# Optimization experiments

Hardware: AMD Instinct MI355X
Metric: run time of the kernel (lower is better)

The kernel has to match this reference:

```python
import jax, jax.numpy as jnp
import numpy as np

N, IN_DIM, OUT_DIM = 8192, 256, 64
NEG_BIG = -9e15
LRELU_SLOPE = 0.01  # torch F.leaky_relu default


def setup_inputs() -> dict:
    key = jax.random.key(0)
    k1, k2, k3, k4 = jax.random.split(key, 4)
    inp = jax.random.normal(k1, (N, IN_DIM), dtype=jnp.float32)
    adj = jax.random.randint(k2, (N, N), 0, 2, dtype=jnp.int32)
    # xavier_uniform with gain=1.414
    limW = 1.414 * np.sqrt(6.0 / (IN_DIM + OUT_DIM))
    W = jax.random.uniform(k3, (IN_DIM, OUT_DIM), minval=-limW, maxval=limW, dtype=jnp.float32)
    lima = 1.414 * np.sqrt(6.0 / (2 * OUT_DIM + 1))
    a = jax.random.uniform(k4, (2 * OUT_DIM, 1), minval=-lima, maxval=lima, dtype=jnp.float32)
    return {"input": inp, "adj": adj, "W": W, "a": a}


def reference(input, adj, W, a):
    h = input @ W                      # [N, D]
    a1, a2 = a[:OUT_DIM, 0], a[OUT_DIM:, 0]
    # e[i,j] = leaky_relu(a1.h_i + a2.h_j) == the concat-based score, no NxNx2D tensor
    f1 = h @ a1                        # [N]
    f2 = h @ a2                        # [N]
    e = jax.nn.leaky_relu(f1[:, None] + f2[None, :], negative_slope=LRELU_SLOPE)  # [N, N]
    face_Rhand = e[1, 2]
    face_Lhand = e[1, 3]
    Rhand_Lhand = e[3, 2]
    attention = jnp.where(adj > 0, e, jnp.float32(NEG_BIG))
    alpha = jax.nn.softmax(attention, axis=1)
    h_prime = alpha @ h                # [N, D]
    return (h_prime, face_Rhand, face_Lhand, Rhand_Lhand)
```

## Files before the change

### kernel.cpp

```cpp
#include <hip/hip_runtime.h>
#include <hip/hip_bf16.h>

#define GN 8192
#define KD 256
#define OD 64
#define LOG2E 1.44269504f
#define ASTR 260
#define NCH 16

typedef __attribute__((ext_vector_type(8))) short bf16x8;
typedef __attribute__((ext_vector_type(4))) float f32x4;

__device__ __forceinline__ float fexp2(float x) {
#if __has_builtin(__builtin_amdgcn_exp2f)
  return __builtin_amdgcn_exp2f(x);
#else
  return exp2f(x);
#endif
}

__global__ __launch_bounds__(256) void gat_k1(
    const float* __restrict__ input, const float* __restrict__ W,
    const float* __restrict__ a, __hip_bfloat16* __restrict__ hTt,
    float* __restrict__ f1p, float* __restrict__ f2p, float* __restrict__ out)
{
  __shared__ float Wl[KD * OD];
  __shared__ float inT[KD * 33];
  __shared__ float red1[8][32];
  __shared__ float red2[8][32];
  __shared__ float s1row[32];
  __shared__ float s2row[32];

  const int tid = threadIdx.x;
  const int i0 = blockIdx.x * 32;

  for (int idx = tid; idx < KD * OD / 4; idx += 256)
    ((float4*)Wl)[idx] = ((const float4*)W)[idx];

#pragma unroll
  for (int it = 0; it < 8; ++it) {
    int idx = tid + it * 256;
    int r = idx >> 6, k4 = idx & 63;
    float4 v = *(const float4*)(input + (long)(i0 + r) * KD + k4 * 4);
    inT[(k4 * 4 + 0) * 33 + r] = v.x;
    inT[(k4 * 4 + 1) * 33 + r] = v.y;
    inT[(k4 * 4 + 2) * 33 + r] = v.z;
    inT[(k4 * 4 + 3) * 33 + r] = v.w;
  }
  __syncthreads();

  const int r = tid & 31;
  const int cg = tid >> 5;
  float acc[8];
#pragma unroll
  for (int c = 0; c < 8; ++c) acc[c] = 0.f;

#pragma unroll 4
  for (int k = 0; k < KD; ++k) {
    float inv = inT[k * 33 + r];
    float4 wa = *(const float4*)&Wl[k * 64 + cg * 8];
    float4 wb = *(const float4*)&Wl[k * 64 + cg * 8 + 4];
    acc[0] += inv * wa.x; acc[1] += inv * wa.y;
    acc[2] += inv * wa.z; acc[3] += inv * wa.w;
    acc[4] += inv * wb.x; acc[5] += inv * wb.y;
    acc[6] += inv * wb.z; acc[7] += inv * wb.w;
  }

#pragma unroll
  for (int c = 0; c < 8; ++c)
    hTt[(long)blockIdx.x * (OD * 32) + (cg * 8 + c) * 32 + r] =
        __float2bfloat16(acc[c]);

  float s1 = 0.f, s2 = 0.f;
#pragma unroll
  for (int c = 0; c < 8; ++c) {
    s1 += acc[c] * a[cg * 8 + c];
    s2 += acc[c] * a[OD + cg * 8 + c];
  }
  red1[cg][r] = s1; red2[cg][r] = s2;
  __syncthreads();
  if (tid < 32) {
    float f1 = 0.f, f2 = 0.f;
#pragma unroll
    for (int g = 0; g < 8; ++g) { f1 += red1[g][tid]; f2 += red2[g][tid]; }
    s1row[tid] = f1; s2row[tid] = f2;
    f1p[i0 + tid] = f1 * LOG2E;
    f2p[i0 + tid] = f2 * LOG2E;
  }
  __syncthreads();
  if (blockIdx.x == 0 && tid == 0) {
    float e12 = s1row[1] + s2row[2];
    float e13 = s1row[1] + s2row[3];
    float e32 = s1row[3] + s2row[2];
    out[(long)GN * OD + 0] = fmaxf(e12, 0.01f * e12);
    out[(long)GN * OD + 1] = fmaxf(e13, 0.01f * e13);
    out[(long)GN * OD + 2] = fmaxf(e32, 0.01f * e32);
  }
}

__global__ __launch_bounds__(256, 3) void gat_k2(
    const int* __restrict__ adj, const __hip_bfloat16* __restrict__ hTt,
    const float* __restrict__ f1p, const float* __restrict__ f2p,
    float* __restrict__ pn, float* __restrict__ pd)
{
  __shared__ int abuf[2][16 * ASTR];
  __shared__ float f2l[4096];
  float* pb = (float*)abuf;
  float* sb = pb + 4 * 16 * 68;

  const int tid = threadIdx.x;
  const int lane = tid & 63;
  const int wv = tid >> 6;
  const int tn = lane & 15;
  const int quad = lane >> 4;
  const int rg = blockIdx.x >> 1;
  const int js = blockIdx.x & 1;
  const int i0 = rg * 16;
  const int jbase = js * 4096;

  for (int i = tid; i < 4096 / 4; i += 256)
    ((float4*)f2l)[i] = ((const float4*)(f2p + jbase))[i];

  const float f1r = f1p[i0 + tn];

  const int sr = tid >> 4;
  const int sc = (tid & 15) * 4;
  const int* gsrc = adj + (long)(i0 + sr) * GN + jbase + sc;

  const int jo0 = wv * 64 + quad * 8;
  const int jo1 = jo0 + 32;
  const __hip_bfloat16* hsl = hTt + (long)(jbase / 32) * (OD * 32) + tn * 32 + quad * 8;

  f32x4 acc[4];
#pragma unroll
  for (int nf = 0; nf < 4; ++nf) acc[nf] = (f32x4){0.f, 0.f, 0.f, 0.f};
  f32x4 accS = (f32x4){0.f, 0.f, 0.f, 0.f};

  bf16x8 ones;
  {
    short ov = (tn == 0) ? (short)0x3F80 : (short)0;
#pragma unroll
    for (int i = 0; i < 8; ++i) ones[i] = ov;
  }

  int4 st[4];
#pragma unroll
  for (int k = 0; k < 4; ++k) st[k] = *(const int4*)(gsrc + 64 * k);
#pragma unroll
  for (int k = 0; k < 4; ++k) *(int4*)&abuf[0][sr * ASTR + sc + 64 * k] = st[k];
  __syncthreads();

  for (int c = 0; c < NCH; ++c) {
    const int cur = c & 1, nxt = cur ^ 1;

    const __hip_bfloat16* h0 = hsl + (long)(c * 8 + 2 * wv) * (OD * 32);
    const __hip_bfloat16* h1 = h0 + (OD * 32);
    bf16x8 B0[4], B1[4];
#pragma unroll
    for (int nf = 0; nf < 4; ++nf) {
      B0[nf] = *(const bf16x8*)(h0 + nf * (16 * 32));
      B1[nf] = *(const bf16x8*)(h1 + nf * (16 * 32));
    }

    if (c + 1 < NCH) {
#pragma unroll
      for (int k = 0; k < 4; ++k)
        st[k] = *(const int4*)(gsrc + (c + 1) * 256 + 64 * k);
    }

    const int4 a0 = *(const int4*)&abuf[cur][tn * ASTR + jo0];
    const int4 a1 = *(const int4*)&abuf[cur][tn * ASTR + jo0 + 4];
    const int4 a2 = *(const int4*)&abuf[cur][tn * ASTR + jo1];
    const int4 a3 = *(const int4*)&abuf[cur][tn * ASTR + jo1 + 4];
    const float4 f20 = *(const float4*)&f2l[c * 256 + jo0];
    const float4 f21 = *(const float4*)&f2l[c * 256 + jo0 + 4];
    const float4 f22 = *(const float4*)&f2l[c * 256 + jo1];
    const float4 f23 = *(const float4*)&f2l[c * 256 + jo1 + 4];

    union { bf16x8 v; unsigned u[4]; } w0, w1;
    {
      float e0 = f1r + f20.x, e1 = f1r + f20.y, e2 = f1r + f20.z, e3 = f1r + f20.w;
      float e4 = f1r + f21.x, e5 = f1r + f21.y, e6 = f1r + f21.z, e7 = f1r + f21.w;
      float v0 = fexp2((a0.x > 0) ? fmaxf(e0, 0.01f * e0) : -256.f);
      float v1 = fexp2((a0.y > 0) ? fmaxf(e1, 0.01f * e1) : -256.f);
      float v2 = fexp2((a0.z > 0) ? fmaxf(e2, 0.01f * e2) : -256.f);
      float v3 = fexp2((a0.w > 0) ? fmaxf(e3, 0.01f * e3) : -256.f);
      float v4 = fexp2((a1.x > 0) ? fmaxf(e4, 0.01f * e4) : -256.f);
      float v5 = fexp2((a1.y > 0) ? fmaxf(e5, 0.01f * e5) : -256.f);
      float v6 = fexp2((a1.z > 0) ? fmaxf(e6, 0.01f * e6) : -256.f);
      float v7 = fexp2((a1.w > 0) ? fmaxf(e7, 0.01f * e7) : -256.f);
      w0.u[0] = __builtin_amdgcn_perm(__float_as_uint(v1), __float_as_uint(v0), 0x07060302u);
      w0.u[1] = __builtin_amdgcn_perm(__float_as_uint(v3), __float_as_uint(v2), 0x07060302u);
      w0.u[2] = __builtin_amdgcn_perm(__float_as_uint(v5), __float_as_uint(v4), 0x07060302u);
      w0.u[3] = __builtin_amdgcn_perm(__float_as_uint(v7), __float_as_uint(v6), 0x07060302u);
    }
    {
      float e0 = f1r + f22.x, e1 = f1r + f22.y, e2 = f1r + f22.z, e3 = f1r + f22.w;
      float e4 = f1r + f23.x, e5 = f1r + f23.y, e6 = f1r + f23.z, e7 = f1r + f23.w;
      float v0 = fexp2((a2.x > 0) ? fmaxf(e0, 0.01f * e0) : -256.f);
      float v1 = fexp2((a2.y > 0) ? fmaxf(e1, 0.01f * e1) : -256.f);
      float v2 = fexp2((a2.z > 0) ? fmaxf(e2, 0.01f * e2) : -256.f);
      float v3 = fexp2((a2.w > 0) ? fmaxf(e3, 0.01f * e3) : -256.f);
      float v4 = fexp2((a3.x > 0) ? fmaxf(e4, 0.01f * e4) : -256.f);
      float v5 = fexp2((a3.y > 0) ? fmaxf(e5, 0.01f * e5) : -256.f);
      float v6 = fexp2((a3.z > 0) ? fmaxf(e6, 0.01f * e6) : -256.f);
      float v7 = fexp2((a3.w > 0) ? fmaxf(e7, 0.01f * e7) : -256.f);
      w1.u[0] = __builtin_amdgcn_perm(__float_as_uint(v1), __float_as_uint(v0), 0x07060302u);
      w1.u[1] = __builtin_amdgcn_perm(__float_as_uint(v3), __float_as_uint(v2), 0x07060302u);
      w1.u[2] = __builtin_amdgcn_perm(__float_as_uint(v5), __float_as_uint(v4), 0x07060302u);
      w1.u[3] = __builtin_amdgcn_perm(__float_as_uint(v7), __float_as_uint(v6), 0x07060302u);
    }

#pragma unroll
    for (int nf = 0; nf < 4; ++nf)
      acc[nf] = __builtin_amdgcn_mfma_f32_16x16x32_bf16(w0.v, B0[nf], acc[nf], 0, 0, 0);
    accS = __builtin_amdgcn_mfma_f32_16x16x32_bf16(w0.v, ones, accS, 0, 0, 0);
#pragma unroll
    for (int nf = 0; nf < 4; ++nf)
      acc[nf] = __builtin_amdgcn_mfma_f32_16x16x32_bf16(w1.v, B1[nf], acc[nf], 0, 0, 0);
    accS = __builtin_amdgcn_mfma_f32_16x16x32_bf16(w1.v, ones, accS, 0, 0, 0);

    if (c + 1 < NCH) {
#pragma unroll
      for (int k = 0; k < 4; ++k)
        *(int4*)&abuf[nxt][sr * ASTR + sc + 64 * k] = st[k];
    }
    __syncthreads();
  }

#pragma unroll
  for (int nf = 0; nf < 4; ++nf)
#pragma unroll
    for (int rgi = 0; rgi < 4; ++rgi)
      pb[(wv * 16 + quad * 4 + rgi) * 68 + nf * 16 + tn] = acc[nf][rgi];
  if (tn == 0) {
#pragma unroll
    for (int rgi = 0; rgi < 4; ++rgi)
      sb[wv * 16 + quad * 4 + rgi] = accS[rgi];
  }
  __syncthreads();
  for (int t = tid; t < 16 * OD; t += 256) {
    int rr = t >> 6, cc = t & 63;
    float num = pb[(0 * 16 + rr) * 68 + cc] + pb[(1 * 16 + rr) * 68 + cc] +
                pb[(2 * 16 + rr) * 68 + cc] + pb[(3 * 16 + rr) * 68 + cc];
    pn[((long)js * GN + i0 + rr) * OD + cc] = num;
  }
  if (tid < 16) {
    float den = sb[0 * 16 + tid] + sb[1 * 16 + tid] + sb[2 * 16 + tid] + sb[3 * 16 + tid];
    pd[(long)js * GN + i0 + tid] = den;
  }
}

__global__ __launch_bounds__(256) void gat_k3(
    const float* __restrict__ pn, const float* __restrict__ pd,
    float* __restrict__ out)
{
  long t = (long)blockIdx.x * 256 + threadIdx.x;
  int i = (int)(t >> 6);
  float num = pn[t] + pn[(long)GN * OD + t];
  float den = pd[i] + pd[GN + i];
  out[t] = num / den;
}

extern "C" void kernel_launch(void* const* d_in, const int* in_sizes, int n_in,
                              void* d_out, int out_size, void* d_ws, size_t ws_size,
                              hipStream_t stream) {
  const float* input = (const float*)d_in[0];
  const int* adj     = (const int*)d_in[1];
  const float* W     = (const float*)d_in[2];
  const float* a     = (const float*)d_in[3];
  float* out = (float*)d_out;

  char* ws = (char*)d_ws;
  __hip_bfloat16* hTt = (__hip_bfloat16*)ws;
  float* f1p = (float*)(ws + (size_t)OD * GN * 2);
  float* f2p = f1p + GN;
  float* pn  = f2p + GN;
  float* pd  = pn + (size_t)2 * GN * OD;

  gat_k1<<<256, 256, 0, stream>>>(input, W, a, hTt, f1p, f2p, out);
  gat_k2<<<1024, 256, 0, stream>>>(adj, hTt, f1p, f2p, pn, pd);
  gat_k3<<<GN * OD / 256, 256, 0, stream>>>(pn, pd, out);
}
```

Measured before the change: 389.7 us.

## Load adjacency directly from global into MFMA layout, drop LDS staging

```diff
diff --git a/kernel.cpp b/kernel.cpp
--- a/kernel.cpp
+++ b/kernel.cpp
@@ -5,7 +5,6 @@
 #define KD 256
 #define OD 64
 #define LOG2E 1.44269504f
-#define ASTR 260
 #define NCH 16
 
 typedef __attribute__((ext_vector_type(8))) short bf16x8;
@@ -98,15 +97,14 @@
   }
 }
 
-__global__ __launch_bounds__(256, 3) void gat_k2(
+__global__ __launch_bounds__(256, 4) void gat_k2(
     const int* __restrict__ adj, const __hip_bfloat16* __restrict__ hTt,
     const float* __restrict__ f1p, const float* __restrict__ f2p,
     float* __restrict__ pn, float* __restrict__ pd)
 {
-  __shared__ int abuf[2][16 * ASTR];
   __shared__ float f2l[4096];
-  float* pb = (float*)abuf;
-  float* sb = pb + 4 * 16 * 68;
+  __shared__ float pb[4 * 16 * 68];
+  __shared__ float sb[64];
 
   const int tid = threadIdx.x;
   const int lane = tid & 63;
@@ -123,12 +121,9 @@
 
   const float f1r = f1p[i0 + tn];
 
-  const int sr = tid >> 4;
-  const int sc = (tid & 15) * 4;
-  const int* gsrc = adj + (long)(i0 + sr) * GN + jbase + sc;
-
   const int jo0 = wv * 64 + quad * 8;
   const int jo1 = jo0 + 32;
+  const int* __restrict__ adjr = adj + (long)(i0 + tn) * GN + jbase;
   const __hip_bfloat16* hsl = hTt + (long)(jbase / 32) * (OD * 32) + tn * 32 + quad * 8;
 
   f32x4 acc[4];
@@ -143,15 +138,14 @@
     for (int i = 0; i < 8; ++i) ones[i] = ov;
   }
 
-  int4 st[4];
-#pragma unroll
-  for (int k = 0; k < 4; ++k) st[k] = *(const int4*)(gsrc + 64 * k);
-#pragma unroll
-  for (int k = 0; k < 4; ++k) *(int4*)&abuf[0][sr * ASTR + sc + 64 * k] = st[k];
   __syncthreads();
 
   for (int c = 0; c < NCH; ++c) {
-    const int cur = c & 1, nxt = cur ^ 1;
+    const int* ap = adjr + c * 256;
+    const int4 a0 = *(const int4*)(ap + jo0);
+    const int4 a1 = *(const int4*)(ap + jo0 + 4);
+    const int4 a2 = *(const int4*)(ap + jo1);
+    const int4 a3 = *(const int4*)(ap + jo1 + 4);
 
     const __hip_bfloat16* h0 = hsl + (long)(c * 8 + 2 * wv) * (OD * 32);
     const __hip_bfloat16* h1 = h0 + (OD * 32);
@@ -162,16 +156,6 @@
       B1[nf] = *(const bf16x8*)(h1 + nf * (16 * 32));
     }
 
-    if (c + 1 < NCH) {
-#pragma unroll
-      for (int k = 0; k < 4; ++k)
-        st[k] = *(const int4*)(gsrc + (c + 1) * 256 + 64 * k);
-    }
-
-    const int4 a0 = *(const int4*)&abuf[cur][tn * ASTR + jo0];
-    const int4 a1 = *(const int4*)&abuf[cur][tn * ASTR + jo0 + 4];
-    const int4 a2 = *(const int4*)&abuf[cur][tn * ASTR + jo1];
-    const int4 a3 = *(const int4*)&abuf[cur][tn * ASTR + jo1 + 4];
     const float4 f20 = *(const float4*)&f2l[c * 256 + jo0];
     const float4 f21 = *(const float4*)&f2l[c * 256 + jo0 + 4];
     const float4 f22 = *(const float4*)&f2l[c * 256 + jo1];
@@ -219,13 +203,6 @@
     for (int nf = 0; nf < 4; ++nf)
       acc[nf] = __builtin_amdgcn_mfma_f32_16x16x32_bf16(w1.v, B1[nf], acc[nf], 0, 0, 0);
     accS = __builtin_amdgcn_mfma_f32_16x16x32_bf16(w1.v, ones, accS, 0, 0, 0);
-
-    if (c + 1 < NCH) {
-#pragma unroll
-      for (int k = 0; k < 4; ++k)
-        *(int4*)&abuf[nxt][sr * ASTR + sc + 64 * k] = st[k];
-    }
-    __syncthreads();
   }
 
 #pragma unroll
```

After: 393.1 us. Within noise of the previous version (+0.9%).
